# Performance work log

Hardware: AMD Instinct MI355X
Metric: run time of the kernel (lower is better)

The kernel has to match this reference:

```python
import jax, jax.numpy as jnp
import numpy as np

B, C, HID, A, K = 128, 2, 150, 8, 30
GRID = 49           # input maze size (forward crops to 49x49)
HP = GRID + 2       # 51: spatial size after kernel=3, padding=2 convs
KS = 3              # value-iteration kernel size


def conv(x, w, b=None, pad=1):
    y = jax.lax.conv_general_dilated(
        x, w, (1, 1), [(pad, pad), (pad, pad)],
        dimension_numbers=('NCHW', 'OIHW', 'NCHW'))
    if b is not None:
        y = y + b[None, :, None, None]
    return y


def unfold9(v):
    # v: [B,1,HP,HP] -> [B,9,HP,HP], 3x3 patches, padding=1 (matches F.unfold)
    vp = jnp.pad(v[:, 0], ((0, 0), (1, 1), (1, 1)))
    return jnp.stack([vp[:, i:i + HP, j:j + HP]
                      for i in range(KS) for j in range(KS)], axis=1)


def setup_inputs() -> dict:
    key = jax.random.key(0)
    ks = jax.random.split(key, 13)
    s = 0.05
    return {
        'grid': (jax.random.uniform(ks[0], (B, C, GRID, GRID)) < 0.3).astype(jnp.float32),
        'x_coord': jax.random.randint(ks[1], (B,), 0, GRID - 2),
        'y_coord': jax.random.randint(ks[2], (B,), 0, GRID - 2),
        'h1_w': jax.random.normal(ks[3], (HID, C, 3, 3)) * s,
        'h1_b': jax.random.normal(ks[4], (HID,)) * s,
        'h2_w': jax.random.normal(ks[5], (HID, HID, 3, 3)) * s,
        'h2_b': jax.random.normal(ks[6], (HID,)) * s,
        'r_w': jax.random.normal(ks[7], (1, HID, 3, 3)) * s,
        't_w': jax.random.normal(ks[8], (A * KS * KS, HID, 3, 3)) * s,
        'a1_w': jax.random.normal(ks[9], (HID, A)) * s,
        'a1_b': jax.random.normal(ks[10], (HID,)) * s,
        'a2_w': jax.random.normal(ks[11], (A, HID)) * s,
        'a2_b': jax.random.normal(ks[12], (A,)) * s,
    }


def reference(grid, x_coord, y_coord, h1_w, h1_b, h2_w, h2_b, r_w, t_w,
              a1_w, a1_b, a2_w, a2_b):
    # hidden feature extractor (padding=1, keeps 49x49)
    h = jax.nn.relu(conv(grid, h1_w, h1_b, pad=1))
    h = jax.nn.relu(conv(h, h2_w, h2_b, pad=1))
    # reward & dynamic transitions (kernel=3, padding=2 -> 51x51)
    reward = conv(h, r_w, None, pad=2)                 # [B,1,51,51]
    trans = conv(h, t_w, None, pad=2)                  # [B,A*9,51,51]
    # softmax over the 9-element kernel dim (loop-invariant in the original)
    sT = jax.nn.softmax(trans.reshape(B, A, KS * KS, HP, HP), axis=2)

    def step(carry, _):
        v, _ = carry
        patches = unfold9(v)                           # [B,9,51,51]
        q = jnp.einsum('bakhw,bkhw->bahw', sT, patches) + reward
        v_new = jnp.max(q, axis=1, keepdims=True)      # [B,1,51,51]
        return (v_new, q), None

    q0 = jnp.zeros((B, A, HP, HP), grid.dtype)
    (v, q_last), _ = jax.lax.scan(step, (jnp.zeros_like(reward), q0),
                                  None, length=K)

    # per-pixel action MLP on cropped q from the LAST iteration
    q_c = q_last[:, :, :GRID, :GRID]                   # [B,A,49,49]
    mid = jax.nn.relu(jnp.einsum('bahw,ca->bchw', q_c, a1_w)
                      + a1_b[None, :, None, None])
    logits = (jnp.einsum('bchw,ac->bahw', mid, a2_w)
              + a2_b[None, :, None, None])             # [B,A,49,49]
    return logits
```

## Files before the change

kernel.cpp:

```cpp
#include <hip/hip_runtime.h>
#include <hip/hip_bf16.h>
#include <stdint.h>

constexpr int NB   = 128;
constexpr int NC   = 2;
constexpr int NH   = 150;
constexpr int NA   = 8;
constexpr int KIT  = 30;
constexpr int GN   = 49;
constexpr int HPN  = 51;
constexpr int NP   = HPN * HPN;
constexpr int RTC  = 73;
constexpr int CIP  = 160;

typedef short v8bf __attribute__((ext_vector_type(8)));
typedef float v4f  __attribute__((ext_vector_type(4)));

__device__ __forceinline__ float bf_lo(uint32_t u){ return __uint_as_float(u << 16); }
__device__ __forceinline__ float bf_hi(uint32_t u){ return __uint_as_float(u & 0xffff0000u); }

__device__ __forceinline__ uint16_t f2bf(float f) {
    uint32_t u = __float_as_uint(f);
    uint32_t lsb = (u >> 16) & 1u;
    u += 0x7fffu + lsb;
    return (uint16_t)(u >> 16);
}

__device__ __forceinline__ float ld_f(const void* p, size_t i, int isbf) {
    if (isbf) {
        uint32_t b = ((const uint16_t*)p)[i];
        return __uint_as_float(b << 16);
    }
    return ((const float*)p)[i];
}
__device__ __forceinline__ uint16_t ld_bf_bits(const void* p, size_t i, int isbf) {
    if (isbf) return ((const uint16_t*)p)[i];
    return f2bf(((const float*)p)[i]);
}

__global__ void detect_kernel(const uint16_t* __restrict__ w, int* __restrict__ flag)
{
    int i = threadIdx.x;
    uint32_t bits = w[2 * i];
    float f = __uint_as_float(bits << 16);
    float a = fabsf(f);
    bool ok = (a >= 1e-10f && a <= 1e5f);
    unsigned long long m = __ballot(ok);
    if (i == 0) flag[0] = (__popcll(m) >= 48) ? 1 : 0;
}

__global__ void prep_kernel(const void* __restrict__ g,
                            const void* __restrict__ w1,
                            const void* __restrict__ b1,
                            const void* __restrict__ w2,
                            const void* __restrict__ b2,
                            const void* __restrict__ rw,
                            const void* __restrict__ tw,
                            const void* __restrict__ a1w,
                            const void* __restrict__ a1b,
                            const void* __restrict__ a2w,
                            const void* __restrict__ a2b,
                            const int* __restrict__ flag,
                            uint16_t* __restrict__ grid_cl,
                            float* __restrict__ wT1, float* __restrict__ bias1,
                            uint16_t* __restrict__ w2t, float* __restrict__ bias2,
                            uint16_t* __restrict__ wrt,
                            float* __restrict__ wA1, float* __restrict__ bA1,
                            float* __restrict__ wA2, float* __restrict__ bA2)
{
    constexpr int N_GRID = NB * GN * GN * NC;
    constexpr int N_WT1  = 9 * NC * NH;
    constexpr int N_B1   = NH;
    constexpr int N_W2T  = 9 * 5 * CIP * 32;
    constexpr int N_B2   = CIP;
    constexpr int N_WRT  = 9 * 5 * 80 * 32;
    constexpr int N_A1W  = NH * NA;
    constexpr int N_A1B  = NH;
    constexpr int N_A2W  = NA * NH;
    constexpr int N_A2B  = NA;

    int isbf = flag[0];
    int i = blockIdx.x * blockDim.x + threadIdx.x;
    if (i < N_GRID) {
        int c = i & 1; int s = (i >> 1) % (GN*GN); int b = i / (GN*GN*2);
        grid_cl[i] = ld_bf_bits(g, (size_t)(b*NC + c)*(GN*GN) + s, isbf);
        return;
    }
    i -= N_GRID;
    if (i < N_WT1) {
        int co = i % NH; int r = i / NH; int ci = r & 1; int k = r >> 1;
        wT1[i] = ld_f(w1, (size_t)co*(NC*9) + ci*9 + k, isbf);
        return;
    }
    i -= N_WT1;
    if (i < N_B1) { bias1[i] = ld_f(b1, i, isbf); return; }
    i -= N_B1;
    if (i < N_W2T) {
        int c  = i % 32;
        int co = (i / 32) % CIP;
        int kc = (i / (32*CIP)) % 5;
        int tap = i / (32*CIP*5);
        int ci = kc*32 + c;
        uint16_t v = 0;
        if (co < NH && ci < NH)
            v = f2bf(ld_f(w2, ((size_t)co*NH + ci)*9 + tap, isbf));
        w2t[i] = v;
        return;
    }
    i -= N_W2T;
    if (i < N_B2) { bias2[i] = (i < NH) ? ld_f(b2, i, isbf) : 0.f; return; }
    i -= N_B2;
    if (i < N_WRT) {
        int c  = i % 32;
        int co = (i / 32) % 80;
        int kc = (i / 2560) % 5;
        int tap = i / 12800;
        int ci = kc*32 + c;
        uint16_t v = 0;
        if (ci < NH) {
            if (co == 0)        v = f2bf(ld_f(rw, (size_t)ci*9 + tap, isbf));
            else if (co <= 72)  v = f2bf(ld_f(tw, ((size_t)(co-1)*NH + ci)*9 + tap, isbf));
        }
        wrt[i] = v;
        return;
    }
    i -= N_WRT;
    if (i < N_A1W) { wA1[i] = ld_f(a1w, i, isbf); return; }
    i -= N_A1W;
    if (i < N_A1B) { bA1[i] = ld_f(a1b, i, isbf); return; }
    i -= N_A1B;
    if (i < N_A2W) { wA2[i] = ld_f(a2w, i, isbf); return; }
    i -= N_A2W;
    if (i < N_A2B) { bA2[i] = ld_f(a2b, i, isbf); return; }
}

__global__ __launch_bounds__(192)
void conv1_cl(const uint16_t* __restrict__ in,
              const float* __restrict__ wT,
              const float* __restrict__ bias,
              uint16_t* __restrict__ out)
{
    constexpr int H = GN, XG = 13;
    int bid = blockIdx.x;
    int xg = bid % XG;
    int y  = (bid / XG) % H;
    int b  = bid / (XG * H);
    int x0 = xg * 4;
    int co = threadIdx.x;

    if (co >= NH) {
        if (co < CIP) {
            #pragma unroll
            for (int xi = 0; xi < 4; ++xi) {
                int x = x0 + xi;
                if (x < H) out[((size_t)(b*H + y)*H + x)*CIP + co] = 0;
            }
        }
        return;
    }

    float bv = bias[co];
    float acc[4] = {bv, bv, bv, bv};

    for (int ky = 0; ky < 3; ++ky) {
        int yy = y + ky - 1;
        if (yy < 0 || yy >= H) continue;
        const uint16_t* rowp = in + (size_t)(b * H + yy) * H * NC;
        #pragma unroll
        for (int kx = 0; kx < 3; ++kx) {
            const float* wp = wT + ((ky*3 + kx) * NC) * NH + co;
            float w0 = wp[0];
            float w1 = wp[NH];
            #pragma unroll
            for (int xi = 0; xi < 4; ++xi) {
                int xx = x0 + xi + kx - 1;
                if (xx < 0 || xx >= H) continue;
                uint32_t u = *(const uint32_t*)(rowp + (size_t)xx * NC);
                acc[xi] += bf_lo(u)*w0 + bf_hi(u)*w1;
            }
        }
    }
    #pragma unroll
    for (int xi = 0; xi < 4; ++xi) {
        int x = x0 + xi;
        if (x < H) out[((size_t)(b*H + y)*H + x)*CIP + co] = f2bf(fmaxf(acc[xi], 0.f));
    }
}

template<int CO_T, int CO_S, int PAD, int OH, bool RELU, bool OBF>
__global__ __launch_bounds__(128)
void conv_mfma(const uint16_t* __restrict__ in,
               const uint16_t* __restrict__ wt,
               const float* __restrict__ bias,
               void* __restrict__ outv)
{
    constexpr int H = GN;
    constexpr int NSUB = CO_S / 16;
    constexpr int CS = CO_T / CO_S;
    constexpr int ASP = 40;
    constexpr int RG = (OH + 7) / 8;
    static_assert(NSUB * 16 == CO_S && CS * CO_S == CO_T, "");

    __shared__ __align__(16) uint16_t shA[10 * 18 * ASP];

    int bid = blockIdx.x;
    int cs = 0;
    if (CS > 1) { cs = bid % CS; bid /= CS; }
    int xg = bid & 3; bid >>= 2;
    int rg = bid % RG;
    int b  = bid / RG;
    int y0 = rg * 8, x0 = xg * 16;
    int co0 = cs * CO_S;
    int t = threadIdx.x;
    int w = t >> 6, l = t & 63;
    int lo16 = l & 15, q4 = l >> 4;

    auto stageHalo = [&](int kc) {
        for (int q = t; q < 720; q += 128) {
            int ci8 = q & 3;
            int c   = (q >> 2) % 18;
            int r   = q / 72;
            int yy = y0 + r - PAD, xx = x0 + c - PAD;
            uint4 v = make_uint4(0u, 0u, 0u, 0u);
            if (yy >= 0 && yy < H && xx >= 0 && xx < H)
                v = *(const uint4*)(in + ((size_t)(b*H + yy)*H + xx)*CIP + kc*32 + ci8*8);
            *(uint4*)(&shA[(r*18 + c)*ASP + ci8*8]) = v;
        }
    };

    const uint16_t* wbase = wt + (size_t)co0*32 + lo16*32 + q4*8;

    v4f acc[4][NSUB];
    #pragma unroll
    for (int si = 0; si < 4; ++si)
        #pragma unroll
        for (int n = 0; n < NSUB; ++n)
            acc[si][n] = (v4f){0.f, 0.f, 0.f, 0.f};

    auto loadB = [&](int sg, v8bf* bf) {
        const uint16_t* p = wbase + (size_t)sg * (CO_T*32);
        #pragma unroll
        for (int n = 0; n < NSUB; ++n)
            bf[n] = *(const v8bf*)(p + n*512);
    };
    auto loadA = [&](int tap, v8bf* af) {
        int ky = tap / 3, kx = tap % 3;
        const uint16_t* base = &shA[((4*w + ky)*18 + lo16 + kx)*ASP + q4*8];
        #pragma unroll
        for (int si = 0; si < 4; ++si)
            af[si] = *(const v8bf*)(base + si*(18*ASP));
    };
    auto compute = [&](v8bf* af, v8bf* bf) {
        #pragma unroll
        for (int n = 0; n < NSUB; ++n) {
            #pragma unroll
            for (int si = 0; si < 4; ++si)
                acc[si][n] = __builtin_amdgcn_mfma_f32_16x16x32_bf16(af[si], bf[n], acc[si][n], 0, 0, 0);
        }
    };

    v8bf bfb[2][NSUB], afb[2][4];
    loadB(0, bfb[0]);
    #pragma unroll
    for (int kc = 0; kc < 5; ++kc) {
        if (kc) __syncthreads();
        stageHalo(kc);
        __syncthreads();
        loadA(0, afb[0]);
        #pragma unroll
        for (int tap = 0; tap < 9; ++tap) {
            int p = (kc * 9 + tap) & 1;
            if (tap < 8) {
                loadB((tap + 1) * 5 + kc, bfb[p ^ 1]);
                loadA(tap + 1, afb[(tap + 1) & 1]);
            } else if (kc < 4) {
                loadB(kc + 1, bfb[p ^ 1]);
            }
            compute(afb[tap & 1], bfb[p]);
        }
    }

    #pragma unroll
    for (int si = 0; si < 4; ++si) {
        int y = y0 + 4*w + si;
        if (y >= OH) continue;
        #pragma unroll
        for (int n = 0; n < NSUB; ++n) {
            int co = co0 + n*16 + lo16;
            float bv = bias ? bias[co] : 0.f;
            #pragma unroll
            for (int r = 0; r < 4; ++r) {
                int x = x0 + q4*4 + r;
                if (x >= OH) continue;
                float v = acc[si][n][r] + bv;
                if (RELU) v = fmaxf(v, 0.f);
                if (OBF) {
                    ((uint16_t*)outv)[((size_t)(b*OH + y)*OH + x)*CIP + co] = f2bf(v);
                } else {
                    if (co < RTC)
                        ((float*)outv)[((size_t)(b*OH + y)*OH + x)*RTC + co] = v;
                }
            }
        }
    }
}

__global__ void softmax_pack_kernel(const float* __restrict__ rt,
                                    uint32_t* __restrict__ sTu,
                                    float* __restrict__ rewb)
{
    int idx = blockIdx.x * blockDim.x + threadIdx.x;
    constexpr int TOT = NB * NP;
    if (idx >= TOT) return;
    const float* tp = rt + (size_t)idx * RTC;
    rewb[idx] = tp[0];
    uint32_t words[36];
    #pragma unroll
    for (int a = 0; a < NA; ++a) {
        const float* s = tp + 1 + a * 9;
        float v[9];
        float m = -1e30f;
        #pragma unroll
        for (int k = 0; k < 9; ++k) { v[k] = s[k]; m = fmaxf(m, v[k]); }
        float sum = 0.f;
        #pragma unroll
        for (int k = 0; k < 9; ++k) { v[k] = expf(v[k] - m); sum += v[k]; }
        float sc = 65535.f / sum;
        #pragma unroll
        for (int k = 0; k < 9; ++k) {
            int gi = a * 9 + k;
            uint32_t u = (uint32_t)__float2uint_rn(v[k] * sc);
            if (gi & 1) words[gi >> 1] |= (u << 16);
            else        words[gi >> 1] = u;
        }
    }
    uint32_t* op = sTu + (size_t)idx * 36;
    #pragma unroll
    for (int j = 0; j < 9; ++j)
        *(uint4*)(op + 4*j) = make_uint4(words[4*j], words[4*j+1], words[4*j+2], words[4*j+3]);
}

__device__ __forceinline__ void vi_pair(const uint32_t* d, const float* pat,
                                        float r, float& qE, float& qO)
{
    float qe = 0.f, qo = 0.f;
    qe = fmaf((float)(d[0] & 0xffffu), pat[0], qe);
    qe = fmaf((float)(d[0] >> 16),     pat[1], qe);
    qe = fmaf((float)(d[1] & 0xffffu), pat[2], qe);
    qe = fmaf((float)(d[1] >> 16),     pat[3], qe);
    qe = fmaf((float)(d[2] & 0xffffu), pat[4], qe);
    qe = fmaf((float)(d[2] >> 16),     pat[5], qe);
    qe = fmaf((float)(d[3] & 0xffffu), pat[6], qe);
    qe = fmaf((float)(d[3] >> 16),     pat[7], qe);
    qe = fmaf((float)(d[4] & 0xffffu), pat[8], qe);
    qo = fmaf((float)(d[4] >> 16),     pat[0], qo);
    qo = fmaf((float)(d[5] & 0xffffu), pat[1], qo);
    qo = fmaf((float)(d[5] >> 16),     pat[2], qo);
    qo = fmaf((float)(d[6] & 0xffffu), pat[3], qo);
    qo = fmaf((float)(d[6] >> 16),     pat[4], qo);
    qo = fmaf((float)(d[7] & 0xffffu), pat[5], qo);
    qo = fmaf((float)(d[7] >> 16),     pat[6], qo);
    qo = fmaf((float)(d[8] & 0xffffu), pat[7], qo);
    qo = fmaf((float)(d[8] >> 16),     pat[8], qo);
    constexpr float inv = 1.f / 65535.f;
    qE = fmaf(qe, inv, r);
    qO = fmaf(qo, inv, r);
}

__global__ __launch_bounds__(1024, 1)
void vi_kernel(const uint32_t* __restrict__ sTu, const float* __restrict__ rewb,
               float* __restrict__ qout)
{
    __shared__ float vb[2][53*53];
    __shared__ float rew[NP];
    int b = blockIdx.x, t = threadIdx.x;
    for (int i = t; i < 53*53; i += 1024) { vb[0][i] = 0.f; vb[1][i] = 0.f; }
    const uint32_t* sb = sTu + (size_t)b * NP * 36;
    for (int i = t; i < NP; i += 1024) rew[i] = rewb[(size_t)b * NP + i];

    int p0 = t, p1 = t + 1024, p2 = t + 2048;
    uint32_t s0[36], s1[36];
    {
        const uint4* a0 = (const uint4*)(sb + (size_t)p0 * 36);
        const uint4* a1 = (const uint4*)(sb + (size_t)p1 * 36);
        #pragma unroll
        for (int j = 0; j < 9; ++j) {
            uint4 v = a0[j];
            s0[4*j+0]=v.x; s0[4*j+1]=v.y; s0[4*j+2]=v.z; s0[4*j+3]=v.w;
            uint4 u = a1[j];
            s1[4*j+0]=u.x; s1[4*j+1]=u.y; s1[4*j+2]=u.z; s1[4*j+3]=u.w;
        }
    }
    __syncthreads();

    float* qb = qout + (size_t)b * NP * NA;
    int cur = 0;
    for (int it = 0; it < KIT; ++it) {
        bool last = (it == KIT - 1);
        const float* vc = vb[cur];
        float* vn = vb[cur ^ 1];
        {
            int y = p0 / HPN, x = p0 % HPN;
            float pat[9];
            #pragma unroll
            for (int dy = 0; dy < 3; ++dy)
                #pragma unroll
                for (int dx = 0; dx < 3; ++dx)
                    pat[dy*3+dx] = vc[(y+dy)*53 + x+dx];
            float r = rew[p0];
            float best = -3.4e38f;
            #pragma unroll
            for (int ap = 0; ap < 4; ++ap) {
                float qE, qO;
                vi_pair(s0 + ap*9, pat, r, qE, qO);
                best = fmaxf(best, fmaxf(qE, qO));
                if (last) {
                    qb[(size_t)p0*NA + 2*ap]     = qE;
                    qb[(size_t)p0*NA + 2*ap + 1] = qO;
                }
            }
            vn[(y+1)*53 + x+1] = best;
        }
        {
            int y = p1 / HPN, x = p1 % HPN;
            float pat[9];
            #pragma unroll
            for (int dy = 0; dy < 3; ++dy)
                #pragma unroll
                for (int dx = 0; dx < 3; ++dx)
                    pat[dy*3+dx] = vc[(y+dy)*53 + x+dx];
            float r = rew[p1];
            float best = -3.4e38f;
            #pragma unroll
            for (int ap = 0; ap < 4; ++ap) {
                float qE, qO;
                vi_pair(s1 + ap*9, pat, r, qE, qO);
                best = fmaxf(best, fmaxf(qE, qO));
                if (last) {
                    qb[(size_t)p1*NA + 2*ap]     = qE;
                    qb[(size_t)p1*NA + 2*ap + 1] = qO;
                }
            }
            vn[(y+1)*53 + x+1] = best;
        }
        if (t < NP - 2048) {
            int y = p2 / HPN, x = p2 % HPN;
            float pat[9];
            #pragma unroll
            for (int dy = 0; dy < 3; ++dy)
                #pragma unroll
                for (int dx = 0; dx < 3; ++dx)
                    pat[dy*3+dx] = vc[(y+dy)*53 + x+dx];
            float r = rew[p2];
            float best = -3.4e38f;
            const uint32_t* gp = sb + (size_t)p2 * 36;
            #pragma unroll
            for (int ap = 0; ap < 4; ++ap) {
                uint32_t d[9];
                #pragma unroll
                for (int j = 0; j < 9; ++j) d[j] = gp[ap*9 + j];
                float qE, qO;
                vi_pair(d, pat, r, qE, qO);
                best = fmaxf(best, fmaxf(qE, qO));
                if (last) {
                    qb[(size_t)p2*NA + 2*ap]     = qE;
                    qb[(size_t)p2*NA + 2*ap + 1] = qO;
                }
            }
            vn[(y+1)*53 + x+1] = best;
        }
        __syncthreads();
        cur ^= 1;
    }
}

__global__ void head_kernel(const float* __restrict__ q,
                            const float* __restrict__ wA1,
                            const float* __restrict__ bA1,
                            const float* __restrict__ wA2,
                            const float* __restrict__ bA2,
                            const int* __restrict__ flag,
                            void* __restrict__ out)
{
    __shared__ float w1[NH*NA], sb1[NH], w2[NA*NH], sb2[NA];
    int t = threadIdx.x;
    for (int i = t; i < NH*NA; i += 256) w1[i] = wA1[i];
    for (int i = t; i < NH;    i += 256) sb1[i] = bA1[i];
    for (int i = t; i < NA*NH; i += 256) w2[i] = wA2[i];
    if (t < NA) sb2[t] = bA2[t];
    __syncthreads();

    int isbf = flag[0];
    int idx = blockIdx.x * 256 + t;
    constexpr int TOT = NB * GN * GN;
    if (idx >= TOT) return;
    int x = idx % GN, y = (idx / GN) % GN, b = idx / (GN*GN);
    const float* qp = q + ((size_t)(b*HPN + y)*HPN + x) * NA;
    float qv[NA];
    #pragma unroll
    for (int a = 0; a < NA; ++a) qv[a] = qp[a];
    float lg[NA];
    #pragma unroll
    for (int a = 0; a < NA; ++a) lg[a] = sb2[a];
    for (int c = 0; c < NH; ++c) {
        float m = sb1[c];
        #pragma unroll
        for (int a = 0; a < NA; ++a) m += qv[a] * w1[c*NA + a];
        m = fmaxf(m, 0.f);
        #pragma unroll
        for (int a = 0; a < NA; ++a) lg[a] += m * w2[a*NH + c];
    }
    #pragma unroll
    for (int a = 0; a < NA; ++a) {
        size_t oi = ((size_t)(b*NA + a)*GN + y)*GN + x;
        float r = lg[a];
        if (isbf) ((uint16_t*)out)[oi] = f2bf(r);
        else      ((float*)out)[oi] = r;
    }
}

extern "C" void kernel_launch(void* const* d_in, const int* in_sizes, int n_in,
                              void* d_out, int out_size, void* d_ws, size_t ws_size,
                              hipStream_t stream)
{
    const void* g   = d_in[0];
    const void* h1w = d_in[3];
    const void* h1b = d_in[4];
    const void* h2w = d_in[5];
    const void* h2b = d_in[6];
    const void* rw  = d_in[7];
    const void* tw  = d_in[8];
    const void* a1w = d_in[9];
    const void* a1b = d_in[10];
    const void* a2w = d_in[11];
    const void* a2b = d_in[12];

    char* ws = (char*)d_ws;
    size_t off = 0;
    auto take = [&](size_t bytes) { size_t r = off; off = (off + bytes + 255) & ~(size_t)255; return r; };

    constexpr size_t N_GRID_CL = (size_t)NB*GN*GN*NC;
    constexpr size_t N_WT1  = 9*NC*NH;
    constexpr size_t N_B1   = NH;
    constexpr size_t N_W2T  = 9*5*CIP*32;
    constexpr size_t N_B2   = CIP;
    constexpr size_t N_WRT  = 9*5*80*32;
    constexpr size_t N_A1W  = NH*NA;
    constexpr size_t N_A1B  = NH;
    constexpr size_t N_A2W  = NA*NH;
    constexpr size_t N_A2B  = NA;
    constexpr size_t N_H    = (size_t)NB*GN*GN*CIP;
    constexpr size_t N_RT   = (size_t)NB*NP*RTC;
    constexpr size_t N_Q    = (size_t)NB*NP*NA;
    constexpr size_t N_STU  = (size_t)NB*NP*36;
    constexpr size_t N_REWB = (size_t)NB*NP;

    size_t off_flag   = take(4);
    size_t off_gridcl = take(N_GRID_CL * 2);
    size_t off_wT1    = take(N_WT1 * 4);
    size_t off_b1     = take(N_B1 * 4);
    size_t off_w2t    = take(N_W2T * 2);
    size_t off_b2     = take(N_B2 * 4);
    size_t off_wrt    = take(N_WRT * 2);
    size_t off_wA1    = take(N_A1W * 4);
    size_t off_bA1    = take(N_A1B * 4);
    size_t off_wA2    = take(N_A2W * 4);
    size_t off_bA2    = take(N_A2B * 4);
    size_t off_q      = take(N_Q * 4);
    size_t szA = (N_RT * 4 > N_H * 2) ? N_RT * 4 : N_H * 2;
    size_t off_A      = take(szA);
    size_t szB = N_H * 2;
    size_t szB2 = ((N_STU * 4 + 255) & ~(size_t)255) + N_REWB * 4;
    if (szB2 > szB) szB = szB2;
    size_t off_B      = take(szB);

    int*      flag    = (int*)(ws + off_flag);
    uint16_t* grid_cl = (uint16_t*)(ws + off_gridcl);
    float*    wT1     = (float*)(ws + off_wT1);
    float*    bias1   = (float*)(ws + off_b1);
    uint16_t* w2t     = (uint16_t*)(ws + off_w2t);
    float*    bias2   = (float*)(ws + off_b2);
    uint16_t* wrt     = (uint16_t*)(ws + off_wrt);
    float*    wA1     = (float*)(ws + off_wA1);
    float*    bA1     = (float*)(ws + off_bA1);
    float*    wA2     = (float*)(ws + off_wA2);
    float*    bA2     = (float*)(ws + off_bA2);
    float*    qbuf    = (float*)(ws + off_q);
    uint16_t* h1      = (uint16_t*)(ws + off_A);
    float*    rt      = (float*)(ws + off_A);
    uint16_t* h2      = (uint16_t*)(ws + off_B);
    uint32_t* sTu     = (uint32_t*)(ws + off_B);
    float*    rewb    = (float*)(ws + off_B + ((N_STU * 4 + 255) & ~(size_t)255));

    detect_kernel<<<1, 64, 0, stream>>>((const uint16_t*)h2w, flag);
    {
        int total = (int)(N_GRID_CL + N_WT1 + N_B1 + N_W2T + N_B2 + N_WRT
                          + N_A1W + N_A1B + N_A2W + N_A2B);
        prep_kernel<<<(total + 255)/256, 256, 0, stream>>>(
            g, h1w, h1b, h2w, h2b, rw, tw, a1w, a1b, a2w, a2b, flag,
            grid_cl, wT1, bias1, w2t, bias2, wrt, wA1, bA1, wA2, bA2);
    }
    conv1_cl<<<NB*GN*13, 192, 0, stream>>>(grid_cl, wT1, bias1, h1);
    conv_mfma<CIP, 80, 1, GN, true, true>
        <<<NB*7*4*2, 128, 0, stream>>>(h1, w2t, bias2, (void*)h2);
    conv_mfma<80, 80, 2, HPN, false, false>
        <<<NB*7*4, 128, 0, stream>>>(h2, wrt, nullptr, (void*)rt);
    softmax_pack_kernel<<<(NB*NP + 255)/256, 256, 0, stream>>>(rt, sTu, rewb);
    vi_kernel<<<NB, 1024, 0, stream>>>(sTu, rewb, qbuf);
    head_kernel<<<(NB*GN*GN + 255)/256, 256, 0, stream>>>(qbuf, wA1, bA1, wA2, bA2, flag,
                                                          d_out);
}
```

Baseline: 1.150 ms.

## Pad activations with zero rings and stage weights in LDS for MFMA convs

Activations h1 and h2 are stored with a zero-padded border, written by a new ring-zeroing kernel, so the MFMA conv kernels can read A fragments straight from global memory with no bounds checks or halo staging. The weights for each input-channel chunk now go into shared memory instead, and blocks grow to 256 threads covering 16x16 output tiles. This removes the per-chunk halo copy and its boundary branches, but every A fragment is now a global load per tap, relying on L1/L2 reuse. Edge rows and columns are clamped, and the shared weight tile is larger.

```diff
diff --git a/kernel.cpp b/kernel.cpp
--- a/kernel.cpp
+++ b/kernel.cpp
@@ -12,6 +12,8 @@
 constexpr int NP   = HPN * HPN;
 constexpr int RTC  = 73;
 constexpr int CIP  = 160;
+constexpr int PD1  = 51;
+constexpr int PD2  = 53;
 
 typedef short v8bf __attribute__((ext_vector_type(8)));
 typedef float v4f  __attribute__((ext_vector_type(4)));
@@ -134,6 +136,32 @@
     if (i < N_A2B) { bA2[i] = ld_f(a2b, i, isbf); return; }
 }
 
+__global__ void zero_ring_kernel(uint16_t* __restrict__ h1p, uint16_t* __restrict__ h2p)
+{
+    int idx = blockIdx.x * 256 + threadIdx.x;
+    constexpr int N1 = NB * 200;
+    constexpr int N2 = NB * 408;
+    uint16_t* dst;
+    if (idx < N1) {
+        int b = idx / 200, cell = idx % 200;
+        int r, c;
+        if (cell < 102) { r = (cell < 51) ? 0 : 50; c = cell % 51; }
+        else { int e = cell - 102; r = 1 + e / 2; c = (e & 1) ? 50 : 0; }
+        dst = h1p + ((size_t)(b*PD1 + r)*PD1 + c)*CIP;
+    } else {
+        idx -= N1;
+        if (idx >= N2) return;
+        int b = idx / 408, cell = idx % 408;
+        int r, c;
+        if (cell < 212) { int rr = cell / 53; r = (rr < 2) ? rr : (49 + rr); c = cell % 53; }
+        else { int e = cell - 212; r = 2 + e / 4; int cc = e & 3; c = (cc < 2) ? cc : (49 + cc); }
+        dst = h2p + ((size_t)(b*PD2 + r)*PD2 + c)*CIP;
+    }
+    uint4 z = make_uint4(0u, 0u, 0u, 0u);
+    #pragma unroll
+    for (int j = 0; j < 20; ++j) *(uint4*)(dst + j*8) = z;
+}
+
 __global__ __launch_bounds__(192)
 void conv1_cl(const uint16_t* __restrict__ in,
               const float* __restrict__ wT,
@@ -153,7 +181,7 @@
             #pragma unroll
             for (int xi = 0; xi < 4; ++xi) {
                 int x = x0 + xi;
-                if (x < H) out[((size_t)(b*H + y)*H + x)*CIP + co] = 0;
+                if (x < H) out[((size_t)(b*PD1 + y+1)*PD1 + (x+1))*CIP + co] = 0;
             }
         }
         return;
@@ -183,52 +211,45 @@
     #pragma unroll
     for (int xi = 0; xi < 4; ++xi) {
         int x = x0 + xi;
-        if (x < H) out[((size_t)(b*H + y)*H + x)*CIP + co] = f2bf(fmaxf(acc[xi], 0.f));
-    }
-}
-
-template<int CO_T, int CO_S, int PAD, int OH, bool RELU, bool OBF>
-__global__ __launch_bounds__(128)
+        if (x < H) out[((size_t)(b*PD1 + y+1)*PD1 + (x+1))*CIP + co] = f2bf(fmaxf(acc[xi], 0.f));
+    }
+}
+
+template<int PD, int CO_T, int CO_S, int PAD, int OH, bool RELU, bool OBF>
+__global__ __launch_bounds__(256)
 void conv_mfma(const uint16_t* __restrict__ in,
                const uint16_t* __restrict__ wt,
                const float* __restrict__ bias,
                void* __restrict__ outv)
 {
-    constexpr int H = GN;
     constexpr int NSUB = CO_S / 16;
     constexpr int CS = CO_T / CO_S;
-    constexpr int ASP = 40;
-    constexpr int RG = (OH + 7) / 8;
     static_assert(NSUB * 16 == CO_S && CS * CO_S == CO_T, "");
-
-    __shared__ __align__(16) uint16_t shA[10 * 18 * ASP];
+    static_assert(PD - 2*PAD == GN - 0 || PD == 2*PAD + 49, "");
+
+    __shared__ __align__(16) uint16_t shB[9 * CO_S * 40];
 
     int bid = blockIdx.x;
     int cs = 0;
     if (CS > 1) { cs = bid % CS; bid /= CS; }
     int xg = bid & 3; bid >>= 2;
-    int rg = bid % RG;
-    int b  = bid / RG;
-    int y0 = rg * 8, x0 = xg * 16;
+    int rg = bid & 3; bid >>= 2;
+    int b  = bid;
+    int y0 = rg * 16, x0 = xg * 16;
     int co0 = cs * CO_S;
     int t = threadIdx.x;
     int w = t >> 6, l = t & 63;
     int lo16 = l & 15, q4 = l >> 4;
 
-    auto stageHalo = [&](int kc) {
-        for (int q = t; q < 720; q += 128) {
-            int ci8 = q & 3;
-            int c   = (q >> 2) % 18;
-            int r   = q / 72;
-            int yy = y0 + r - PAD, xx = x0 + c - PAD;
-            uint4 v = make_uint4(0u, 0u, 0u, 0u);
-            if (yy >= 0 && yy < H && xx >= 0 && xx < H)
-                v = *(const uint4*)(in + ((size_t)(b*H + yy)*H + xx)*CIP + kc*32 + ci8*8);
-            *(uint4*)(&shA[(r*18 + c)*ASP + ci8*8]) = v;
-        }
-    };
-
-    const uint16_t* wbase = wt + (size_t)co0*32 + lo16*32 + q4*8;
+    int xi = x0 + lo16;
+    int xic = min(xi, OH - 1);
+    const uint16_t* pb[4];
+    #pragma unroll
+    for (int si = 0; si < 4; ++si) {
+        int yr = y0 + 4*w + si;
+        int yc = min(yr, OH - 1);
+        pb[si] = in + ((size_t)(b*PD + yc)*PD + xic)*CIP + q4*8;
+    }
 
     v4f acc[4][NSUB];
     #pragma unroll
@@ -237,46 +258,40 @@
         for (int n = 0; n < NSUB; ++n)
             acc[si][n] = (v4f){0.f, 0.f, 0.f, 0.f};
 
-    auto loadB = [&](int sg, v8bf* bf) {
-        const uint16_t* p = wbase + (size_t)sg * (CO_T*32);
-        #pragma unroll
-        for (int n = 0; n < NSUB; ++n)
-            bf[n] = *(const v8bf*)(p + n*512);
-    };
-    auto loadA = [&](int tap, v8bf* af) {
-        int ky = tap / 3, kx = tap % 3;
-        const uint16_t* base = &shA[((4*w + ky)*18 + lo16 + kx)*ASP + q4*8];
-        #pragma unroll
-        for (int si = 0; si < 4; ++si)
-            af[si] = *(const v8bf*)(base + si*(18*ASP));
-    };
-    auto compute = [&](v8bf* af, v8bf* bf) {
-        #pragma unroll
-        for (int n = 0; n < NSUB; ++n) {
-            #pragma unroll
-            for (int si = 0; si < 4; ++si)
-                acc[si][n] = __builtin_amdgcn_mfma_f32_16x16x32_bf16(af[si], bf[n], acc[si][n], 0, 0, 0);
-        }
-    };
-
-    v8bf bfb[2][NSUB], afb[2][4];
-    loadB(0, bfb[0]);
+    v8bf afb[2][4];
     #pragma unroll
     for (int kc = 0; kc < 5; ++kc) {
         if (kc) __syncthreads();
-        stageHalo(kc);
+        for (int q = t; q < 9*CO_S*4; q += 256) {
+            int ci8 = q & 3;
+            int co  = (q >> 2) % CO_S;
+            int tap = q / (CO_S*4);
+            uint4 v = *(const uint4*)(wt + (((size_t)tap*5 + kc)*CO_T + co0 + co)*32 + ci8*8);
+            *(uint4*)(&shB[(tap*CO_S + co)*40 + ci8*8]) = v;
+        }
         __syncthreads();
-        loadA(0, afb[0]);
+
+        #pragma unroll
+        for (int si = 0; si < 4; ++si)
+            afb[0][si] = *(const v8bf*)(pb[si] + kc*32);
         #pragma unroll
         for (int tap = 0; tap < 9; ++tap) {
-            int p = (kc * 9 + tap) & 1;
             if (tap < 8) {
-                loadB((tap + 1) * 5 + kc, bfb[p ^ 1]);
-                loadA(tap + 1, afb[(tap + 1) & 1]);
-            } else if (kc < 4) {
-                loadB(kc + 1, bfb[p ^ 1]);
-            }
-            compute(afb[tap & 1], bfb[p]);
+                int ky = (tap+1) / 3, kx = (tap+1) % 3;
+                #pragma unroll
+                for (int si = 0; si < 4; ++si)
+                    afb[(tap+1) & 1][si] = *(const v8bf*)(pb[si] + kc*32 + (ky*PD + kx)*CIP);
+            }
+            v8bf bf[NSUB];
+            #pragma unroll
+            for (int n = 0; n < NSUB; ++n)
+                bf[n] = *(const v8bf*)(&shB[(tap*CO_S + n*16 + lo16)*40 + q4*8]);
+            #pragma unroll
+            for (int n = 0; n < NSUB; ++n) {
+                #pragma unroll
+                for (int si = 0; si < 4; ++si)
+                    acc[si][n] = __builtin_amdgcn_mfma_f32_16x16x32_bf16(afb[tap & 1][si], bf[n], acc[si][n], 0, 0, 0);
+            }
         }
     }
 
@@ -295,7 +310,7 @@
                 float v = acc[si][n][r] + bv;
                 if (RELU) v = fmaxf(v, 0.f);
                 if (OBF) {
-                    ((uint16_t*)outv)[((size_t)(b*OH + y)*OH + x)*CIP + co] = f2bf(v);
+                    ((uint16_t*)outv)[((size_t)(b*PD2 + y+2)*PD2 + (x+2))*CIP + co] = f2bf(v);
                 } else {
                     if (co < RTC)
                         ((float*)outv)[((size_t)(b*OH + y)*OH + x)*RTC + co] = v;
@@ -549,7 +564,8 @@
     constexpr size_t N_A1B  = NH;
     constexpr size_t N_A2W  = NA*NH;
     constexpr size_t N_A2B  = NA;
-    constexpr size_t N_H    = (size_t)NB*GN*GN*CIP;
+    constexpr size_t N_H1P  = (size_t)NB*PD1*PD1*CIP;
+    constexpr size_t N_H2P  = (size_t)NB*PD2*PD2*CIP;
     constexpr size_t N_RT   = (size_t)NB*NP*RTC;
     constexpr size_t N_Q    = (size_t)NB*NP*NA;
     constexpr size_t N_STU  = (size_t)NB*NP*36;
@@ -567,9 +583,9 @@
     size_t off_wA2    = take(N_A2W * 4);
     size_t off_bA2    = take(N_A2B * 4);
     size_t off_q      = take(N_Q * 4);
-    size_t szA = (N_RT * 4 > N_H * 2) ? N_RT * 4 : N_H * 2;
+    size_t szA = (N_RT * 4 > N_H1P * 2) ? N_RT * 4 : N_H1P * 2;
     size_t off_A      = take(szA);
-    size_t szB = N_H * 2;
+    size_t szB = N_H2P * 2;
     size_t szB2 = ((N_STU * 4 + 255) & ~(size_t)255) + N_REWB * 4;
     if (szB2 > szB) szB = szB2;
     size_t off_B      = take(szB);
@@ -586,9 +602,9 @@
     float*    wA2     = (float*)(ws + off_wA2);
     float*    bA2     = (float*)(ws + off_bA2);
     float*    qbuf    = (float*)(ws + off_q);
-    uint16_t* h1      = (uint16_t*)(ws + off_A);
+    uint16_t* h1p     = (uint16_t*)(ws + off_A);
     float*    rt      = (float*)(ws + off_A);
-    uint16_t* h2      = (uint16_t*)(ws + off_B);
+    uint16_t* h2p     = (uint16_t*)(ws + off_B);
     uint32_t* sTu     = (uint32_t*)(ws + off_B);
     float*    rewb    = (float*)(ws + off_B + ((N_STU * 4 + 255) & ~(size_t)255));
 
@@ -600,11 +616,12 @@
             g, h1w, h1b, h2w, h2b, rw, tw, a1w, a1b, a2w, a2b, flag,
             grid_cl, wT1, bias1, w2t, bias2, wrt, wA1, bA1, wA2, bA2);
     }
-    conv1_cl<<<NB*GN*13, 192, 0, stream>>>(grid_cl, wT1, bias1, h1);
-    conv_mfma<CIP, 80, 1, GN, true, true>
-        <<<NB*7*4*2, 128, 0, stream>>>(h1, w2t, bias2, (void*)h2);
-    conv_mfma<80, 80, 2, HPN, false, false>
-        <<<NB*7*4, 128, 0, stream>>>(h2, wrt, nullptr, (void*)rt);
+    zero_ring_kernel<<<(NB*(200+408) + 255)/256, 256, 0, stream>>>(h1p, h2p);
+    conv1_cl<<<NB*GN*13, 192, 0, stream>>>(grid_cl, wT1, bias1, h1p);
+    conv_mfma<PD1, CIP, 80, 1, GN, true, true>
+        <<<NB*4*4*2, 256, 0, stream>>>(h1p, w2t, bias2, (void*)h2p);
+    conv_mfma<PD2, 80, 80, 2, HPN, false, false>
+        <<<NB*4*4, 256, 0, stream>>>(h2p, wrt, nullptr, (void*)rt);
     softmax_pack_kernel<<<(NB*NP + 255)/256, 256, 0, stream>>>(rt, sTu, rewb);
     vi_kernel<<<NB, 1024, 0, stream>>>(sTu, rewb, qbuf);
     head_kernel<<<(NB*GN*GN + 255)/256, 256, 0, stream>>>(qbuf, wA1, bA1, wA2, bA2, flag,
```

After: 1.235 ms. 7.3% more time.

## Enlarge conv MFMA tiles to 12 rows with 3 waves and stage weights in LDS

Applied to the files above, without the earlier changes.

The implicit-GEMM conv kernel now processes 12 output rows per block using 192 threads (3 waves), which cuts halo overhead and block count. Weights are staged cooperatively into shared memory in groups of three taps instead of each lane loading them directly from global memory. The old register double-buffering of A and B fragments is removed, and extra barriers are added per tap group. This trades software prefetch overlap for more data reuse and fewer redundant global weight reads.

```diff
diff --git a/kernel.cpp b/kernel.cpp
--- a/kernel.cpp
+++ b/kernel.cpp
@@ -188,7 +188,7 @@
 }
 
 template<int CO_T, int CO_S, int PAD, int OH, bool RELU, bool OBF>
-__global__ __launch_bounds__(128)
+__global__ __launch_bounds__(192)
 void conv_mfma(const uint16_t* __restrict__ in,
                const uint16_t* __restrict__ wt,
                const float* __restrict__ bias,
@@ -197,11 +197,13 @@
     constexpr int H = GN;
     constexpr int NSUB = CO_S / 16;
     constexpr int CS = CO_T / CO_S;
-    constexpr int ASP = 40;
-    constexpr int RG = (OH + 7) / 8;
+    constexpr int HR = 12 + 2*PAD;
+    constexpr int HC = 16 + 2*PAD;
+    constexpr int RG = (OH + 11) / 12;
     static_assert(NSUB * 16 == CO_S && CS * CO_S == CO_T, "");
 
-    __shared__ __align__(16) uint16_t shA[10 * 18 * ASP];
+    __shared__ __align__(16) uint16_t shA[HR * HC * 40];
+    __shared__ __align__(16) uint16_t shB[3 * CO_S * 40];
 
     int bid = blockIdx.x;
     int cs = 0;
@@ -209,26 +211,34 @@
     int xg = bid & 3; bid >>= 2;
     int rg = bid % RG;
     int b  = bid / RG;
-    int y0 = rg * 8, x0 = xg * 16;
+    int y0 = rg * 12, x0 = xg * 16;
     int co0 = cs * CO_S;
     int t = threadIdx.x;
     int w = t >> 6, l = t & 63;
     int lo16 = l & 15, q4 = l >> 4;
 
-    auto stageHalo = [&](int kc) {
-        for (int q = t; q < 720; q += 128) {
+    auto stageA = [&](int kc) {
+        for (int q = t; q < HR*HC*4; q += 192) {
             int ci8 = q & 3;
-            int c   = (q >> 2) % 18;
-            int r   = q / 72;
+            int c   = (q >> 2) % HC;
+            int r   = (q >> 2) / HC;
             int yy = y0 + r - PAD, xx = x0 + c - PAD;
             uint4 v = make_uint4(0u, 0u, 0u, 0u);
             if (yy >= 0 && yy < H && xx >= 0 && xx < H)
                 v = *(const uint4*)(in + ((size_t)(b*H + yy)*H + xx)*CIP + kc*32 + ci8*8);
-            *(uint4*)(&shA[(r*18 + c)*ASP + ci8*8]) = v;
+            *(uint4*)(&shA[(r*HC + c)*40 + ci8*8]) = v;
         }
     };
-
-    const uint16_t* wbase = wt + (size_t)co0*32 + lo16*32 + q4*8;
+    auto stageB = [&](int kc, int tg) {
+        for (int q = t; q < 3*CO_S*4; q += 192) {
+            int ci8 = q & 3;
+            int co  = (q >> 2) % CO_S;
+            int tip = (q >> 2) / CO_S;
+            int tap = tg*3 + tip;
+            uint4 v = *(const uint4*)(wt + (((size_t)tap*5 + kc)*CO_T + co0 + co)*32 + ci8*8);
+            *(uint4*)(&shB[(tip*CO_S + co)*40 + ci8*8]) = v;
+        }
+    };
 
     v4f acc[4][NSUB];
     #pragma unroll
@@ -237,46 +247,32 @@
         for (int n = 0; n < NSUB; ++n)
             acc[si][n] = (v4f){0.f, 0.f, 0.f, 0.f};
 
-    auto loadB = [&](int sg, v8bf* bf) {
-        const uint16_t* p = wbase + (size_t)sg * (CO_T*32);
-        #pragma unroll
-        for (int n = 0; n < NSUB; ++n)
-            bf[n] = *(const v8bf*)(p + n*512);
-    };
-    auto loadA = [&](int tap, v8bf* af) {
-        int ky = tap / 3, kx = tap % 3;
-        const uint16_t* base = &shA[((4*w + ky)*18 + lo16 + kx)*ASP + q4*8];
-        #pragma unroll
-        for (int si = 0; si < 4; ++si)
-            af[si] = *(const v8bf*)(base + si*(18*ASP));
-    };
-    auto compute = [&](v8bf* af, v8bf* bf) {
-        #pragma unroll
-        for (int n = 0; n < NSUB; ++n) {
-            #pragma unroll
-            for (int si = 0; si < 4; ++si)
-                acc[si][n] = __builtin_amdgcn_mfma_f32_16x16x32_bf16(af[si], bf[n], acc[si][n], 0, 0, 0);
-        }
-    };
-
-    v8bf bfb[2][NSUB], afb[2][4];
-    loadB(0, bfb[0]);
-    #pragma unroll
     for (int kc = 0; kc < 5; ++kc) {
-        if (kc) __syncthreads();
-        stageHalo(kc);
         __syncthreads();
-        loadA(0, afb[0]);
-        #pragma unroll
-        for (int tap = 0; tap < 9; ++tap) {
-            int p = (kc * 9 + tap) & 1;
-            if (tap < 8) {
-                loadB((tap + 1) * 5 + kc, bfb[p ^ 1]);
-                loadA(tap + 1, afb[(tap + 1) & 1]);
-            } else if (kc < 4) {
-                loadB(kc + 1, bfb[p ^ 1]);
-            }
-            compute(afb[tap & 1], bfb[p]);
+        stageA(kc);
+        stageB(kc, 0);
+        __syncthreads();
+        #pragma unroll
+        for (int tg = 0; tg < 3; ++tg) {
+            if (tg) {
+                __syncthreads();
+                stageB(kc, tg);
+                __syncthreads();
+            }
+            #pragma unroll
+            for (int tip = 0; tip < 3; ++tip) {
+                v8bf af[4];
+                #pragma unroll
+                for (int si = 0; si < 4; ++si)
+                    af[si] = *(const v8bf*)(&shA[((4*w + si + tg)*HC + lo16 + tip)*40 + q4*8]);
+                #pragma unroll
+                for (int n = 0; n < NSUB; ++n) {
+                    v8bf bf = *(const v8bf*)(&shB[(tip*CO_S + n*16 + lo16)*40 + q4*8]);
+                    #pragma unroll
+                    for (int si = 0; si < 4; ++si)
+                        acc[si][n] = __builtin_amdgcn_mfma_f32_16x16x32_bf16(af[si], bf, acc[si][n], 0, 0, 0);
+                }
+            }
         }
     }
 
@@ -602,9 +598,9 @@
     }
     conv1_cl<<<NB*GN*13, 192, 0, stream>>>(grid_cl, wT1, bias1, h1);
     conv_mfma<CIP, 80, 1, GN, true, true>
-        <<<NB*7*4*2, 128, 0, stream>>>(h1, w2t, bias2, (void*)h2);
+        <<<NB*5*4*2, 192, 0, stream>>>(h1, w2t, bias2, (void*)h2);
     conv_mfma<80, 80, 2, HPN, false, false>
-        <<<NB*7*4, 128, 0, stream>>>(h2, wrt, nullptr, (void*)rt);
+        <<<NB*5*4, 192, 0, stream>>>(h2, wrt, nullptr, (void*)rt);
     softmax_pack_kernel<<<(NB*NP + 255)/256, 256, 0, stream>>>(rt, sTu, rewb);
     vi_kernel<<<NB, 1024, 0, stream>>>(sTu, rewb, qbuf);
     head_kernel<<<(NB*GN*GN + 255)/256, 256, 0, stream>>>(qbuf, wA1, bA1, wA2, bA2, flag,
```

New measurement: 1.311 ms. 14.0% more time.
